# Optimization experiments

Measured on AMD Instinct MI355X. Metric: run time of the kernel, lower is better.

The kernel has to match this reference:

```python
import jax, jax.numpy as jnp
import numpy as np

B, S, K, N, G = 4, 16, 8192, 8192, 128
NUM_GROUPS = K // G

def setup_inputs() -> dict:
    key = jax.random.key(0)
    k1, k2, k3, k4, k5 = jax.random.split(key, 5)
    x = jax.random.normal(k1, (B, S, K), dtype=jnp.float32)
    qweight = jax.random.randint(k2, (K, N), -128, 128, dtype=jnp.int32)
    # small positive scales like real quantizers produce
    scales = jax.random.uniform(k3, (NUM_GROUPS, N), dtype=jnp.float32) * 0.01 + 1e-4
    zeros = jax.random.uniform(k4, (NUM_GROUPS, N), dtype=jnp.float32) * 2.0 - 1.0
    bias = jax.random.normal(k5, (N,), dtype=jnp.float32)
    return {"x": x, "qweight": qweight, "scales": scales, "zeros": zeros,
            "bias": bias, "group_size": G}

def reference(x, qweight, scales, zeros, bias, group_size):
    # Expand per-group scale/zero along K: [num_groups, N] -> [K, N]
    Kdim = qweight.shape[0]
    if scales.shape[0] == 1:
        scale_exp = jnp.broadcast_to(scales, (Kdim, scales.shape[1]))
        zero_exp = jnp.broadcast_to(zeros, (Kdim, zeros.shape[1]))
    else:
        scale_exp = jnp.repeat(scales, group_size, axis=0)[:Kdim]
        zero_exp = jnp.repeat(zeros, group_size, axis=0)[:Kdim]
    # Dequantize: W[k, n] = (q - zero) * scale
    weight_fp = (qweight.astype(x.dtype) - zero_exp) * scale_exp  # [K, N]
    out = jnp.einsum('bsk,kn->bsn', x, weight_fp) + bias
    return out
```

## Files before the change

kernel.cpp:

```cpp
#include <hip/hip_runtime.h>

typedef __attribute__((ext_vector_type(8))) short short8;
typedef __attribute__((ext_vector_type(8))) unsigned short ushort8;
typedef __attribute__((ext_vector_type(4))) unsigned short ushort4v;
typedef __attribute__((ext_vector_type(4))) int int4v;
typedef __attribute__((ext_vector_type(4))) float f32x4;

#define Mdim 64
#define Kdim 8192
#define Ndim 8192
#define GRP 128
#define NGRP 64
#define KSPLIT 4
#define NG2 (NGRP / KSPLIT)
#define BN 128

#define SWZ(row, kk) ((row)*128 + ((kk) ^ (8*((((row) >> 3) ^ (row)) & 7))))

__device__ __forceinline__ unsigned short f2bf(float f) {
    unsigned int u = __builtin_bit_cast(unsigned int, f);
    u += 0x7FFFu + ((u >> 16) & 1u);
    return (unsigned short)(u >> 16);
}
__device__ __forceinline__ float bf2f(unsigned short h) {
    unsigned int u = ((unsigned int)h) << 16;
    return __builtin_bit_cast(float, u);
}

__global__ void prep_kernel(const float* __restrict__ x,
                            unsigned short* __restrict__ xh,
                            unsigned short* __restrict__ xl,
                            float* __restrict__ xsum) {
    const int tid = threadIdx.x;
    const int u = blockIdx.x * 8 + (tid >> 5);
    const int g = u & (NGRP - 1);
    const int m = u >> 6;
    const int lane = tid & 31;
    const int k = g * GRP + lane * 4;
    f32x4 v = *(const f32x4*)(x + (size_t)m * Kdim + k);
    ushort4v hv, lv;
    float s = 0.f;
#pragma unroll
    for (int i = 0; i < 4; ++i) {
        unsigned short h = f2bf(v[i]);
        hv[i] = h;
        lv[i] = f2bf(v[i] - bf2f(h));
        s += v[i];
    }
    *(ushort4v*)(xh + (size_t)m * Kdim + k) = hv;
    *(ushort4v*)(xl + (size_t)m * Kdim + k) = lv;
#pragma unroll
    for (int off = 16; off > 0; off >>= 1) s += __shfl_down(s, off, 32);
    if (lane == 0) xsum[g * Mdim + m] = s;
}

__launch_bounds__(512)
__global__ void qlin_kernel(const unsigned short* __restrict__ xh,
                            const unsigned short* __restrict__ xl,
                            const int* __restrict__ qw,
                            const float* __restrict__ scales,
                            const float* __restrict__ zeros,
                            const float* __restrict__ xsum,
                            float* __restrict__ pout) {
    __shared__ unsigned short lq[2][128 * 128];
    __shared__ unsigned short lxh[64 * 128];
    __shared__ unsigned short lxl[64 * 128];

    const int tid = threadIdx.x;
    const int kh = blockIdx.x & (KSPLIT - 1);
    const int n0 = (blockIdx.x >> 2) * BN;
    const int g0 = kh * NG2;
    const int ph = ((blockIdx.x >> 2) & 1) * (NG2 / 2);

    const int w = tid >> 6;
    const int l = tid & 63;
    const int lcol = l & 15;
    const int lhi = l >> 4;

    const int qc = tid & 31;
    const int qr = tid >> 5;
    const int xc = tid & 15;
    const int xm = tid >> 4;

    const int nn = n0 + w * 16 + lcol;

    int4v qv[8];
    ushort8 xga, xgb, xgc, xgd;
    float s_n, z_n, s_c, z_c;
    f32x4 xs_n[4], xs_c[4];

    auto LOAD_SZX = [&](int g) {
        s_n = scales[(size_t)g * Ndim + nn];
        z_n = zeros[(size_t)g * Ndim + nn];
#pragma unroll
        for (int mf = 0; mf < 4; ++mf)
            xs_n[mf] = *(const f32x4*)(xsum + g * Mdim + mf * 16 + lhi * 4);
    };
    auto LOADX = [&](int g) {
        const size_t kb = (size_t)g * GRP + xc * 8;
        xga = *(const ushort8*)(xh + (size_t)xm * Kdim + kb);
        xgb = *(const ushort8*)(xh + (size_t)(xm + 32) * Kdim + kb);
        xgc = *(const ushort8*)(xl + (size_t)xm * Kdim + kb);
        xgd = *(const ushort8*)(xl + (size_t)(xm + 32) * Kdim + kb);
    };
    auto LOADQ = [&](int g) {
        const size_t kb = (size_t)g * GRP + qr * 8;
        const int nc = n0 + qc * 4;
#pragma unroll
        for (int j = 0; j < 8; ++j)
            qv[j] = *(const int4v*)(qw + (kb + j) * Ndim + nc);
    };
    auto WRITEX = [&]() {
        *(ushort8*)&lxh[SWZ(xm, xc * 8)] = xga;
        *(ushort8*)&lxh[SWZ(xm + 32, xc * 8)] = xgb;
        *(ushort8*)&lxl[SWZ(xm, xc * 8)] = xgc;
        *(ushort8*)&lxl[SWZ(xm + 32, xc * 8)] = xgd;
    };
    auto WRITEQ = [&](int bb) {
#pragma unroll
        for (int i = 0; i < 4; ++i) {
            int4v pk;
#pragma unroll
            for (int t = 0; t < 4; ++t) {
                unsigned lo = __builtin_bit_cast(unsigned, (float)qv[2 * t][i]) >> 16;
                unsigned hi = __builtin_bit_cast(unsigned, (float)qv[2 * t + 1][i]) & 0xFFFF0000u;
                pk[t] = (int)(lo | hi);
            }
            *(int4v*)&lq[bb][SWZ(qc * 4 + i, qr * 8)] = pk;
        }
    };

    f32x4 acc[4];
#pragma unroll
    for (int mf = 0; mf < 4; ++mf) acc[mf] = {0.f, 0.f, 0.f, 0.f};

    auto COMPUTE = [&](int bb) {
        short8 bq[4];
#pragma unroll
        for (int ks = 0; ks < 4; ++ks)
            bq[ks] = *(const short8*)&lq[bb][SWZ(w * 16 + lcol, ks * 32 + lhi * 8)];
#pragma unroll
        for (int mf = 0; mf < 4; ++mf) {
            short8 ah[4], al[4];
#pragma unroll
            for (int ks = 0; ks < 4; ++ks) {
                ah[ks] = *(const short8*)&lxh[SWZ(mf * 16 + lcol, ks * 32 + lhi * 8)];
                al[ks] = *(const short8*)&lxl[SWZ(mf * 16 + lcol, ks * 32 + lhi * 8)];
            }
            f32x4 p = {0.f, 0.f, 0.f, 0.f};
#pragma unroll
            for (int ks = 0; ks < 4; ++ks) {
                p = __builtin_amdgcn_mfma_f32_16x16x32_bf16(ah[ks], bq[ks], p, 0, 0, 0);
                p = __builtin_amdgcn_mfma_f32_16x16x32_bf16(al[ks], bq[ks], p, 0, 0, 0);
            }
#pragma unroll
            for (int r = 0; r < 4; ++r)
                acc[mf][r] += s_c * (p[r] - z_c * xs_c[mf][r]);
        }
    };

    {
        const int ga = g0 + ph;
        LOAD_SZX(ga);
        LOADX(ga);
        LOADQ(ga);
        s_c = s_n; z_c = z_n;
#pragma unroll
        for (int mf = 0; mf < 4; ++mf) xs_c[mf] = xs_n[mf];
        WRITEX();
        WRITEQ(0);
        __syncthreads();
    }

    for (int g = 0; g < NG2; ++g) {
        const int bb = g & 1;
        const bool more = (g + 1 < NG2);

        if (more) {
            const int ga = g0 + ((g + 1 + ph) & (NG2 - 1));
            LOAD_SZX(ga);
            LOADX(ga);
            LOADQ(ga);
        }

        COMPUTE(bb);

        if (more) {
            __syncthreads();
            WRITEQ(bb ^ 1);
            s_c = s_n; z_c = z_n;
#pragma unroll
            for (int mf = 0; mf < 4; ++mf) xs_c[mf] = xs_n[mf];
            WRITEX();
            __syncthreads();
        }
    }

    const size_t ob = (size_t)kh * Mdim * Ndim;
#pragma unroll
    for (int mf = 0; mf < 4; ++mf)
#pragma unroll
        for (int r = 0; r < 4; ++r)
            pout[ob + (size_t)(mf * 16 + lhi * 4 + r) * Ndim + nn] = acc[mf][r];
}

__global__ void reduce_kernel(const float* __restrict__ pout,
                              const float* __restrict__ bias,
                              float* __restrict__ out) {
    const size_t e = ((size_t)blockIdx.x * 256 + threadIdx.x) * 4;
    const int n = (int)(e & (Ndim - 1));
    f32x4 a = *(const f32x4*)(bias + n);
#pragma unroll
    for (int s = 0; s < KSPLIT; ++s) {
        f32x4 ppart = *(const f32x4*)(pout + (size_t)s * Mdim * Ndim + e);
#pragma unroll
        for (int r = 0; r < 4; ++r) a[r] += ppart[r];
    }
    *(f32x4*)(out + e) = a;
}

extern "C" void kernel_launch(void* const* d_in, const int* in_sizes, int n_in,
                              void* d_out, int out_size, void* d_ws, size_t ws_size,
                              hipStream_t stream) {
    const float* x = (const float*)d_in[0];
    const int* qw = (const int*)d_in[1];
    const float* scales = (const float*)d_in[2];
    const float* zeros = (const float*)d_in[3];
    const float* bias = (const float*)d_in[4];

    unsigned short* xh = (unsigned short*)d_ws;
    unsigned short* xl = xh + (size_t)Mdim * Kdim;
    float* xsum = (float*)(xl + (size_t)Mdim * Kdim);
    float* pout = xsum + NGRP * Mdim;
    float* out = (float*)d_out;

    prep_kernel<<<512, 256, 0, stream>>>(x, xh, xl, xsum);
    qlin_kernel<<<(Ndim / BN) * KSPLIT, 512, 0, stream>>>(xh, xl, qw, scales, zeros, xsum, pout);
    reduce_kernel<<<(Mdim * Ndim / 4) / 256, 256, 0, stream>>>(pout, bias, out);
}
```

Before: 66.70 us.

## Double K-split, 2x2 warp tiling, single LDS buffer, stage scales in LDS

Raises the K split from 4 to 8, doubling the grid to 512 blocks, and adds a min-blocks hint to launch_bounds so more blocks fit per CU. Each warp now computes a 32x32 tile (2x2 MFMA fragments) instead of 16x64, which reuses each loaded A/B fragment across two MFMAs. The LDS weight buffer drops from double to single buffering, and per-group scales, zeros and x-sums are preloaded once into shared memory instead of fetched from global each group. The aim is better occupancy and fewer LDS reads. The cost is twice as much partial-output traffic into the reduce kernel, and reads of the single shared buffer must now finish before it is refilled.

```diff
diff --git a/kernel.cpp b/kernel.cpp
--- a/kernel.cpp
+++ b/kernel.cpp
@@ -11,7 +11,7 @@
 #define Ndim 8192
 #define GRP 128
 #define NGRP 64
-#define KSPLIT 4
+#define KSPLIT 8
 #define NG2 (NGRP / KSPLIT)
 #define BN 128
 
@@ -54,7 +54,7 @@
     if (lane == 0) xsum[g * Mdim + m] = s;
 }
 
-__launch_bounds__(512)
+__launch_bounds__(512, 4)
 __global__ void qlin_kernel(const unsigned short* __restrict__ xh,
                             const unsigned short* __restrict__ xl,
                             const int* __restrict__ qw,
@@ -62,40 +62,37 @@
                             const float* __restrict__ zeros,
                             const float* __restrict__ xsum,
                             float* __restrict__ pout) {
-    __shared__ unsigned short lq[2][128 * 128];
+    __shared__ unsigned short lq[128 * 128];
     __shared__ unsigned short lxh[64 * 128];
     __shared__ unsigned short lxl[64 * 128];
+    __shared__ float ls[NG2][128];
+    __shared__ float lz[NG2][128];
+    __shared__ float lxs[NG2][64];
 
     const int tid = threadIdx.x;
     const int kh = blockIdx.x & (KSPLIT - 1);
-    const int n0 = (blockIdx.x >> 2) * BN;
+    const int n0 = (blockIdx.x >> 3) * BN;
     const int g0 = kh * NG2;
-    const int ph = ((blockIdx.x >> 2) & 1) * (NG2 / 2);
+    const int ph = ((blockIdx.x >> 8) & 1) * (NG2 / 2);
 
     const int w = tid >> 6;
     const int l = tid & 63;
     const int lcol = l & 15;
     const int lhi = l >> 4;
+    const int mt = (w >> 2) * 32;
+    const int ns = (w & 3) * 32;
 
     const int qc = tid & 31;
     const int qr = tid >> 5;
     const int xc = tid & 15;
     const int xm = tid >> 4;
 
-    const int nn = n0 + w * 16 + lcol;
+    const int c0 = n0 + ns + lcol;
+    const int c1 = c0 + 16;
 
     int4v qv[8];
     ushort8 xga, xgb, xgc, xgd;
-    float s_n, z_n, s_c, z_c;
-    f32x4 xs_n[4], xs_c[4];
-
-    auto LOAD_SZX = [&](int g) {
-        s_n = scales[(size_t)g * Ndim + nn];
-        z_n = zeros[(size_t)g * Ndim + nn];
-#pragma unroll
-        for (int mf = 0; mf < 4; ++mf)
-            xs_n[mf] = *(const f32x4*)(xsum + g * Mdim + mf * 16 + lhi * 4);
-    };
+
     auto LOADX = [&](int g) {
         const size_t kb = (size_t)g * GRP + xc * 8;
         xga = *(const ushort8*)(xh + (size_t)xm * Kdim + kb);
@@ -116,7 +113,7 @@
         *(ushort8*)&lxl[SWZ(xm, xc * 8)] = xgc;
         *(ushort8*)&lxl[SWZ(xm + 32, xc * 8)] = xgd;
     };
-    auto WRITEQ = [&](int bb) {
+    auto WRITEQ = [&]() {
 #pragma unroll
         for (int i = 0; i < 4; ++i) {
             int4v pk;
@@ -126,82 +123,89 @@
                 unsigned hi = __builtin_bit_cast(unsigned, (float)qv[2 * t + 1][i]) & 0xFFFF0000u;
                 pk[t] = (int)(lo | hi);
             }
-            *(int4v*)&lq[bb][SWZ(qc * 4 + i, qr * 8)] = pk;
-        }
-    };
-
-    f32x4 acc[4];
-#pragma unroll
-    for (int mf = 0; mf < 4; ++mf) acc[mf] = {0.f, 0.f, 0.f, 0.f};
-
-    auto COMPUTE = [&](int bb) {
-        short8 bq[4];
-#pragma unroll
-        for (int ks = 0; ks < 4; ++ks)
-            bq[ks] = *(const short8*)&lq[bb][SWZ(w * 16 + lcol, ks * 32 + lhi * 8)];
-#pragma unroll
-        for (int mf = 0; mf < 4; ++mf) {
-            short8 ah[4], al[4];
-#pragma unroll
-            for (int ks = 0; ks < 4; ++ks) {
-                ah[ks] = *(const short8*)&lxh[SWZ(mf * 16 + lcol, ks * 32 + lhi * 8)];
-                al[ks] = *(const short8*)&lxl[SWZ(mf * 16 + lcol, ks * 32 + lhi * 8)];
-            }
-            f32x4 p = {0.f, 0.f, 0.f, 0.f};
-#pragma unroll
-            for (int ks = 0; ks < 4; ++ks) {
-                p = __builtin_amdgcn_mfma_f32_16x16x32_bf16(ah[ks], bq[ks], p, 0, 0, 0);
-                p = __builtin_amdgcn_mfma_f32_16x16x32_bf16(al[ks], bq[ks], p, 0, 0, 0);
-            }
-#pragma unroll
-            for (int r = 0; r < 4; ++r)
-                acc[mf][r] += s_c * (p[r] - z_c * xs_c[mf][r]);
-        }
-    };
-
+            *(int4v*)&lq[SWZ(qc * 4 + i, qr * 8)] = pk;
+        }
+    };
+
+    f32x4 acc00 = {0,0,0,0}, acc01 = {0,0,0,0}, acc10 = {0,0,0,0}, acc11 = {0,0,0,0};
+
+    if (tid < 256) {
+        *(f32x4*)&ls[tid >> 5][(tid & 31) * 4] =
+            *(const f32x4*)(scales + (size_t)(g0 + (tid >> 5)) * Ndim + n0 + (tid & 31) * 4);
+    } else {
+        const int t = tid - 256;
+        *(f32x4*)&lz[t >> 5][(t & 31) * 4] =
+            *(const f32x4*)(zeros + (size_t)(g0 + (t >> 5)) * Ndim + n0 + (t & 31) * 4);
+    }
+    lxs[tid >> 6][tid & 63] = xsum[(g0 + (tid >> 6)) * Mdim + (tid & 63)];
     {
         const int ga = g0 + ph;
-        LOAD_SZX(ga);
         LOADX(ga);
         LOADQ(ga);
-        s_c = s_n; z_c = z_n;
-#pragma unroll
-        for (int mf = 0; mf < 4; ++mf) xs_c[mf] = xs_n[mf];
         WRITEX();
-        WRITEQ(0);
+        WRITEQ();
         __syncthreads();
     }
 
     for (int g = 0; g < NG2; ++g) {
-        const int bb = g & 1;
+        const int gi = (g + ph) & (NG2 - 1);
         const bool more = (g + 1 < NG2);
 
         if (more) {
             const int ga = g0 + ((g + 1 + ph) & (NG2 - 1));
-            LOAD_SZX(ga);
             LOADX(ga);
             LOADQ(ga);
         }
 
-        COMPUTE(bb);
+        f32x4 p00 = {0,0,0,0}, p01 = {0,0,0,0}, p10 = {0,0,0,0}, p11 = {0,0,0,0};
+#pragma unroll
+        for (int ks = 0; ks < 4; ++ks) {
+            const int kk = ks * 32 + lhi * 8;
+            short8 bq0 = *(const short8*)&lq[SWZ(ns + lcol, kk)];
+            short8 bq1 = *(const short8*)&lq[SWZ(ns + 16 + lcol, kk)];
+            short8 ah0 = *(const short8*)&lxh[SWZ(mt + lcol, kk)];
+            short8 al0 = *(const short8*)&lxl[SWZ(mt + lcol, kk)];
+            short8 ah1 = *(const short8*)&lxh[SWZ(mt + 16 + lcol, kk)];
+            short8 al1 = *(const short8*)&lxl[SWZ(mt + 16 + lcol, kk)];
+            p00 = __builtin_amdgcn_mfma_f32_16x16x32_bf16(ah0, bq0, p00, 0, 0, 0);
+            p00 = __builtin_amdgcn_mfma_f32_16x16x32_bf16(al0, bq0, p00, 0, 0, 0);
+            p01 = __builtin_amdgcn_mfma_f32_16x16x32_bf16(ah0, bq1, p01, 0, 0, 0);
+            p01 = __builtin_amdgcn_mfma_f32_16x16x32_bf16(al0, bq1, p01, 0, 0, 0);
+            p10 = __builtin_amdgcn_mfma_f32_16x16x32_bf16(ah1, bq0, p10, 0, 0, 0);
+            p10 = __builtin_amdgcn_mfma_f32_16x16x32_bf16(al1, bq0, p10, 0, 0, 0);
+            p11 = __builtin_amdgcn_mfma_f32_16x16x32_bf16(ah1, bq1, p11, 0, 0, 0);
+            p11 = __builtin_amdgcn_mfma_f32_16x16x32_bf16(al1, bq1, p11, 0, 0, 0);
+        }
+        {
+            const float s0 = ls[gi][ns + lcol],      z0 = lz[gi][ns + lcol];
+            const float s1 = ls[gi][ns + 16 + lcol], z1 = lz[gi][ns + 16 + lcol];
+            f32x4 xs0 = *(const f32x4*)&lxs[gi][mt + lhi * 4];
+            f32x4 xs1 = *(const f32x4*)&lxs[gi][mt + 16 + lhi * 4];
+#pragma unroll
+            for (int r = 0; r < 4; ++r) {
+                acc00[r] += s0 * (p00[r] - z0 * xs0[r]);
+                acc01[r] += s1 * (p01[r] - z1 * xs0[r]);
+                acc10[r] += s0 * (p10[r] - z0 * xs1[r]);
+                acc11[r] += s1 * (p11[r] - z1 * xs1[r]);
+            }
+        }
 
         if (more) {
             __syncthreads();
-            WRITEQ(bb ^ 1);
-            s_c = s_n; z_c = z_n;
-#pragma unroll
-            for (int mf = 0; mf < 4; ++mf) xs_c[mf] = xs_n[mf];
             WRITEX();
+            WRITEQ();
             __syncthreads();
         }
     }
 
     const size_t ob = (size_t)kh * Mdim * Ndim;
 #pragma unroll
-    for (int mf = 0; mf < 4; ++mf)
-#pragma unroll
-        for (int r = 0; r < 4; ++r)
-            pout[ob + (size_t)(mf * 16 + lhi * 4 + r) * Ndim + nn] = acc[mf][r];
+    for (int r = 0; r < 4; ++r) {
+        pout[ob + (size_t)(mt + lhi * 4 + r) * Ndim + c0] = acc00[r];
+        pout[ob + (size_t)(mt + lhi * 4 + r) * Ndim + c1] = acc01[r];
+        pout[ob + (size_t)(mt + 16 + lhi * 4 + r) * Ndim + c0] = acc10[r];
+        pout[ob + (size_t)(mt + 16 + lhi * 4 + r) * Ndim + c1] = acc11[r];
+    }
 }
 
 __global__ void reduce_kernel(const float* __restrict__ pout,
```

Result: faster. 61.53 us (-7.8%).
